# Kernel optimization log

Measured on AMD Instinct MI355X. Metric: run time of the kernel, lower is better.

Reference implementation:

```python
import jax, jax.numpy as jnp
import numpy as np

EPS = 1e-5  # torch BatchNorm1d default eps


def setup_inputs() -> dict:
    key = jax.random.key(0)
    ks = jax.random.split(key, 8)
    B, H, D, DO = 8192, 8, 512, 256
    return {
        "x_concepts_encoded": jax.random.normal(ks[0], (B, H, D), dtype=jnp.float32),
        "relevance_weights": jax.random.uniform(ks[1], (B, H), dtype=jnp.float32),
        "bn_gamma": jax.random.uniform(ks[2], (D,), dtype=jnp.float32) + 0.5,
        "bn_beta": jax.random.normal(ks[3], (D,), dtype=jnp.float32) * 0.1,
        "bn_mean": jax.random.normal(ks[4], (D,), dtype=jnp.float32) * 0.1,
        "bn_var": jax.random.uniform(ks[5], (D,), dtype=jnp.float32) + 0.5,
        "W": jax.random.normal(ks[6], (DO, D), dtype=jnp.float32) / np.sqrt(D),
        "b": jax.random.normal(ks[7], (DO,), dtype=jnp.float32) * 0.01,
    }


def reference(x_concepts_encoded, relevance_weights, bn_gamma, bn_beta, bn_mean, bn_var, W, b):
    B, H = relevance_weights.shape
    x = x_concepts_encoded.reshape(B * H, -1)            # [B*H, D]
    # BatchNorm1d (inference: running stats) fused as scale/shift
    inv = bn_gamma * jax.lax.rsqrt(bn_var + EPS)
    h = x * inv + (bn_beta - bn_mean * inv)              # [B*H, D]
    # Swish
    h = h * jax.nn.sigmoid(h)
    # Linear
    out = h @ W.T + b                                    # [B*H, DO]
    # relevance-weighted sum over heads
    out = jnp.einsum('bhd,bh->bd', out.reshape(B, H, -1), relevance_weights)
    return out
```

## Files before the change

### kernel.cpp

```cpp
#include <hip/hip_runtime.h>
#include <hip/hip_bf16.h>

#define NB 8192
#define NH 8
#define ND 512
#define NO 256
#define ROWS 32
#define TPB 512

typedef __attribute__((ext_vector_type(8))) short short8;
typedef __attribute__((ext_vector_type(4))) float f32x4;

__device__ __align__(16) ushort g_wb[NO * ND];

__device__ __forceinline__ ushort f2bf(float f) {
    union { float f; unsigned u; } v; v.f = f;
    unsigned u = v.u;
    unsigned r = u + 0x7FFFu + ((u >> 16) & 1u);
    return (ushort)(r >> 16);
}

__global__ __launch_bounds__(256) void wcvt_kernel(const float* __restrict__ W) {
    int i = (blockIdx.x * 256 + threadIdx.x) * 4;
    float4 w = *(const float4*)(W + i);
    ushort4 o;
    o.x = f2bf(w.x); o.y = f2bf(w.y); o.z = f2bf(w.z); o.w = f2bf(w.w);
    *(ushort4*)(g_wb + i) = o;
}

__device__ __forceinline__ float swishf(float h) {
    return h * __builtin_amdgcn_rcpf(1.0f + __expf(-h));
}

__global__ __launch_bounds__(TPB) void fused_kernel(
    const float* __restrict__ x, const float* __restrict__ rw,
    const float* __restrict__ gamma, const float* __restrict__ beta,
    const float* __restrict__ mean, const float* __restrict__ var,
    const float* __restrict__ bias, float* __restrict__ out)
{
    __shared__ __align__(16) ushort yl[ROWS * ND];
    __shared__ float rwl[ROWS * NH];

    const int tid = threadIdx.x;
    const int b0  = blockIdx.x * ROWS;
    const int d4  = tid & 127;
    const int rh  = tid >> 7;
    const int d   = d4 * 4;

    const int lane = tid & 63;
    const int wv   = tid >> 6;
    const int n0   = wv * 32;
    const int lr   = lane & 15;
    const int lk   = (lane >> 4) * 8;

    if (tid < 64)
        ((float4*)rwl)[tid] = ((const float4*)(rw + (size_t)b0 * NH))[tid];

    float4 g4 = *(const float4*)(gamma + d);
    float4 v4 = *(const float4*)(var   + d);
    float4 be = *(const float4*)(beta  + d);
    float4 me = *(const float4*)(mean  + d);
    const float ix = g4.x * rsqrtf(v4.x + 1e-5f);
    const float iy = g4.y * rsqrtf(v4.y + 1e-5f);
    const float iz = g4.z * rsqrtf(v4.z + 1e-5f);
    const float iw = g4.w * rsqrtf(v4.w + 1e-5f);
    const float ox = be.x - me.x * ix;
    const float oy = be.y - me.y * iy;
    const float oz = be.z - me.z * iz;
    const float ow = be.w - me.w * iw;

    __syncthreads();

    #pragma unroll
    for (int it = 0; it < 8; ++it) {
        const int rr = rh + it * 4;
        const float* xr = x + (size_t)(b0 + rr) * (NH * ND) + d;
        const float4 w0 = ((const float4*)(rwl + rr * NH))[0];
        const float4 w1 = ((const float4*)(rwl + rr * NH))[1];
        const float whv[NH] = {w0.x, w0.y, w0.z, w0.w, w1.x, w1.y, w1.z, w1.w};

        float ax = 0.f, ay = 0.f, az = 0.f, aw = 0.f;
        #pragma unroll
        for (int h = 0; h < NH; ++h) {
            float4 xa = *(const float4*)(xr + h * ND);
            const float wh = whv[h];
            ax += wh * swishf(xa.x * ix + ox);
            ay += wh * swishf(xa.y * iy + oy);
            az += wh * swishf(xa.z * iz + oz);
            aw += wh * swishf(xa.w * iw + ow);
        }
        const int addr = rr * 1024 + ((d * 2) ^ ((rr & 7) << 4));
        ushort4 o;
        o.x = f2bf(ax); o.y = f2bf(ay); o.z = f2bf(az); o.w = f2bf(aw);
        *(ushort4*)((char*)yl + addr) = o;
    }

    const ushort* wp = g_wb + (size_t)(n0 + lr) * ND + lk;
    short8 rb0[4], rb1[4];
    #pragma unroll
    for (int p = 0; p < 4; ++p) {
        rb0[p] = *(const short8*)(wp + p * 32);
        rb1[p] = *(const short8*)(wp + 16 * ND + p * 32);
    }
    __builtin_amdgcn_sched_barrier(0);
    __syncthreads();

    f32x4 acc00 = {0.f,0.f,0.f,0.f};
    f32x4 acc01 = {0.f,0.f,0.f,0.f};
    f32x4 acc10 = {0.f,0.f,0.f,0.f};
    f32x4 acc11 = {0.f,0.f,0.f,0.f};

    const char* ylb0 = (const char*)yl + lr * 1024;
    const char* ylb1 = (const char*)yl + (lr + 16) * 1024;
    const int swz = (lr & 7) << 4;

    #pragma unroll
    for (int ks = 0; ks < 16; ++ks) {
        short8 b0 = rb0[ks & 3];
        short8 b1 = rb1[ks & 3];
        if (ks + 4 < 16) {
            rb0[ks & 3] = *(const short8*)(wp + (ks + 4) * 32);
            rb1[ks & 3] = *(const short8*)(wp + 16 * ND + (ks + 4) * 32);
        }
        const int kb = (ks * 32 + lk) * 2;
        short8 a0 = *(const short8*)(ylb0 + (kb ^ swz));
        short8 a1 = *(const short8*)(ylb1 + (kb ^ swz));
        acc00 = __builtin_amdgcn_mfma_f32_16x16x32_bf16(a0, b0, acc00, 0, 0, 0);
        acc01 = __builtin_amdgcn_mfma_f32_16x16x32_bf16(a0, b1, acc01, 0, 0, 0);
        acc10 = __builtin_amdgcn_mfma_f32_16x16x32_bf16(a1, b0, acc10, 0, 0, 0);
        acc11 = __builtin_amdgcn_mfma_f32_16x16x32_bf16(a1, b1, acc11, 0, 0, 0);
    }

    const int rbase = (lane >> 4) * 4;
    float sw0[4], sw1[4];
    #pragma unroll
    for (int q = 0; q < 4; ++q) {
        const float* rp0 = rwl + (rbase + q) * NH;
        const float* rp1 = rwl + (16 + rbase + q) * NH;
        sw0[q] = ((rp0[0]+rp0[1]) + (rp0[2]+rp0[3])) + ((rp0[4]+rp0[5]) + (rp0[6]+rp0[7]));
        sw1[q] = ((rp1[0]+rp1[1]) + (rp1[2]+rp1[3])) + ((rp1[4]+rp1[5]) + (rp1[6]+rp1[7]));
    }
    f32x4 accs0[2] = {acc00, acc01};
    f32x4 accs1[2] = {acc10, acc11};
    #pragma unroll
    for (int nf = 0; nf < 2; ++nf) {
        const int col = n0 + nf * 16 + lr;
        const float bn = bias[col];
        #pragma unroll
        for (int q = 0; q < 4; ++q) {
            const int r = rbase + q;
            out[(size_t)(b0 + r) * NO + col]      = accs0[nf][q] + bn * sw0[q];
            out[(size_t)(b0 + 16 + r) * NO + col] = accs1[nf][q] + bn * sw1[q];
        }
    }
}

extern "C" void kernel_launch(void* const* d_in, const int* in_sizes, int n_in,
                              void* d_out, int out_size, void* d_ws, size_t ws_size,
                              hipStream_t stream) {
    const float* x     = (const float*)d_in[0];
    const float* rw    = (const float*)d_in[1];
    const float* gamma = (const float*)d_in[2];
    const float* beta  = (const float*)d_in[3];
    const float* mean  = (const float*)d_in[4];
    const float* var   = (const float*)d_in[5];
    const float* W     = (const float*)d_in[6];
    const float* bias  = (const float*)d_in[7];
    float* out = (float*)d_out;

    hipLaunchKernelGGL(wcvt_kernel, dim3((NO * ND) / 1024), dim3(256), 0, stream, W);
    hipLaunchKernelGGL(fused_kernel, dim3(NB / ROWS), dim3(TPB), 0, stream,
                       x, rw, gamma, beta, mean, var, bias, out);
}
```

Baseline: 38.24 us.

## Split block work into two half-row phases overlapping x loads with MFMA

Splits each block's 32 rows into two halves. The first 16 rows are reduced and multiplied, while global loads for the second half's x rows are already in flight before the first MFMA loop starts. The second half's swish and reduce and its own MFMA pass follow. The aim is to hide HBM latency for x behind the first GEMM, at the cost of reloading the W fragments, an extra barrier and higher register pressure from holding 16 prefetched float4s.

```diff
diff --git a/kernel.cpp b/kernel.cpp
--- a/kernel.cpp
+++ b/kernel.cpp
@@ -71,28 +71,37 @@
 
     __syncthreads();
 
-    #pragma unroll
-    for (int it = 0; it < 8; ++it) {
+#define COMPUTE_FROM(Xb, rr) do {                                           \
+    const float4 _w0 = ((const float4*)(rwl + (rr) * NH))[0];               \
+    const float4 _w1 = ((const float4*)(rwl + (rr) * NH))[1];               \
+    const float _whv[NH] = {_w0.x,_w0.y,_w0.z,_w0.w,_w1.x,_w1.y,_w1.z,_w1.w};\
+    float ax = 0.f, ay = 0.f, az = 0.f, aw = 0.f;                           \
+    _Pragma("unroll")                                                       \
+    for (int h = 0; h < NH; ++h) {                                          \
+        const float _wh = _whv[h];                                          \
+        ax += _wh * swishf(Xb[h].x * ix + ox);                              \
+        ay += _wh * swishf(Xb[h].y * iy + oy);                              \
+        az += _wh * swishf(Xb[h].z * iz + oz);                              \
+        aw += _wh * swishf(Xb[h].w * iw + ow);                              \
+    }                                                                       \
+    const int _addr = (rr) * 1024 + ((d * 2) ^ (((rr) & 7) << 4));          \
+    ushort4 _o;                                                             \
+    _o.x = f2bf(ax); _o.y = f2bf(ay); _o.z = f2bf(az); _o.w = f2bf(aw);     \
+    *(ushort4*)((char*)yl + _addr) = _o;                                    \
+} while (0)
+
+#define ISSUE(Xb, rr) do {                                                  \
+    const float* _xr = x + (size_t)(b0 + (rr)) * (NH * ND) + d;             \
+    _Pragma("unroll")                                                       \
+    for (int h = 0; h < NH; ++h) Xb[h] = *(const float4*)(_xr + h * ND);    \
+} while (0)
+
+    #pragma unroll
+    for (int it = 0; it < 4; ++it) {
         const int rr = rh + it * 4;
-        const float* xr = x + (size_t)(b0 + rr) * (NH * ND) + d;
-        const float4 w0 = ((const float4*)(rwl + rr * NH))[0];
-        const float4 w1 = ((const float4*)(rwl + rr * NH))[1];
-        const float whv[NH] = {w0.x, w0.y, w0.z, w0.w, w1.x, w1.y, w1.z, w1.w};
-
-        float ax = 0.f, ay = 0.f, az = 0.f, aw = 0.f;
-        #pragma unroll
-        for (int h = 0; h < NH; ++h) {
-            float4 xa = *(const float4*)(xr + h * ND);
-            const float wh = whv[h];
-            ax += wh * swishf(xa.x * ix + ox);
-            ay += wh * swishf(xa.y * iy + oy);
-            az += wh * swishf(xa.z * iz + oz);
-            aw += wh * swishf(xa.w * iw + ow);
-        }
-        const int addr = rr * 1024 + ((d * 2) ^ ((rr & 7) << 4));
-        ushort4 o;
-        o.x = f2bf(ax); o.y = f2bf(ay); o.z = f2bf(az); o.w = f2bf(aw);
-        *(ushort4*)((char*)yl + addr) = o;
+        float4 Xc[NH];
+        ISSUE(Xc, rr);
+        COMPUTE_FROM(Xc, rr);
     }
 
     const ushort* wp = g_wb + (size_t)(n0 + lr) * ND + lk;
@@ -102,16 +111,17 @@
         rb0[p] = *(const short8*)(wp + p * 32);
         rb1[p] = *(const short8*)(wp + 16 * ND + p * 32);
     }
+
+    float4 X0[NH], X1[NH];
+    ISSUE(X0, 16 + rh);
+    ISSUE(X1, 16 + rh + 4);
+
     __builtin_amdgcn_sched_barrier(0);
     __syncthreads();
 
-    f32x4 acc00 = {0.f,0.f,0.f,0.f};
-    f32x4 acc01 = {0.f,0.f,0.f,0.f};
-    f32x4 acc10 = {0.f,0.f,0.f,0.f};
-    f32x4 acc11 = {0.f,0.f,0.f,0.f};
-
+    f32x4 accA = {0.f,0.f,0.f,0.f};
+    f32x4 accB = {0.f,0.f,0.f,0.f};
     const char* ylb0 = (const char*)yl + lr * 1024;
-    const char* ylb1 = (const char*)yl + (lr + 16) * 1024;
     const int swz = (lr & 7) << 4;
 
     #pragma unroll
@@ -124,35 +134,82 @@
         }
         const int kb = (ks * 32 + lk) * 2;
         short8 a0 = *(const short8*)(ylb0 + (kb ^ swz));
+        accA = __builtin_amdgcn_mfma_f32_16x16x32_bf16(a0, b0, accA, 0, 0, 0);
+        accB = __builtin_amdgcn_mfma_f32_16x16x32_bf16(a0, b1, accB, 0, 0, 0);
+    }
+
+    const int rbase = (lane >> 4) * 4;
+    {
+        float sw0[4];
+        #pragma unroll
+        for (int q = 0; q < 4; ++q) {
+            const float* rp = rwl + (rbase + q) * NH;
+            sw0[q] = ((rp[0]+rp[1]) + (rp[2]+rp[3])) + ((rp[4]+rp[5]) + (rp[6]+rp[7]));
+        }
+        f32x4 accs[2] = {accA, accB};
+        #pragma unroll
+        for (int nf = 0; nf < 2; ++nf) {
+            const int col = n0 + nf * 16 + lr;
+            const float bn = bias[col];
+            #pragma unroll
+            for (int q = 0; q < 4; ++q)
+                out[(size_t)(b0 + rbase + q) * NO + col] = accs[nf][q] + bn * sw0[q];
+        }
+    }
+
+    COMPUTE_FROM(X0, 16 + rh);
+    ISSUE(X0, 16 + rh + 8);
+    COMPUTE_FROM(X1, 16 + rh + 4);
+    ISSUE(X1, 16 + rh + 12);
+    COMPUTE_FROM(X0, 16 + rh + 8);
+    COMPUTE_FROM(X1, 16 + rh + 12);
+
+    #pragma unroll
+    for (int p = 0; p < 4; ++p) {
+        rb0[p] = *(const short8*)(wp + p * 32);
+        rb1[p] = *(const short8*)(wp + 16 * ND + p * 32);
+    }
+    __builtin_amdgcn_sched_barrier(0);
+    __syncthreads();
+
+    f32x4 accC = {0.f,0.f,0.f,0.f};
+    f32x4 accD = {0.f,0.f,0.f,0.f};
+    const char* ylb1 = (const char*)yl + (lr + 16) * 1024;
+
+    #pragma unroll
+    for (int ks = 0; ks < 16; ++ks) {
+        short8 b0 = rb0[ks & 3];
+        short8 b1 = rb1[ks & 3];
+        if (ks + 4 < 16) {
+            rb0[ks & 3] = *(const short8*)(wp + (ks + 4) * 32);
+            rb1[ks & 3] = *(const short8*)(wp + 16 * ND + (ks + 4) * 32);
+        }
+        const int kb = (ks * 32 + lk) * 2;
         short8 a1 = *(const short8*)(ylb1 + (kb ^ swz));
-        acc00 = __builtin_amdgcn_mfma_f32_16x16x32_bf16(a0, b0, acc00, 0, 0, 0);
-        acc01 = __builtin_amdgcn_mfma_f32_16x16x32_bf16(a0, b1, acc01, 0, 0, 0);
-        acc10 = __builtin_amdgcn_mfma_f32_16x16x32_bf16(a1, b0, acc10, 0, 0, 0);
-        acc11 = __builtin_amdgcn_mfma_f32_16x16x32_bf16(a1, b1, acc11, 0, 0, 0);
-    }
-
-    const int rbase = (lane >> 4) * 4;
-    float sw0[4], sw1[4];
-    #pragma unroll
-    for (int q = 0; q < 4; ++q) {
-        const float* rp0 = rwl + (rbase + q) * NH;
-        const float* rp1 = rwl + (16 + rbase + q) * NH;
-        sw0[q] = ((rp0[0]+rp0[1]) + (rp0[2]+rp0[3])) + ((rp0[4]+rp0[5]) + (rp0[6]+rp0[7]));
-        sw1[q] = ((rp1[0]+rp1[1]) + (rp1[2]+rp1[3])) + ((rp1[4]+rp1[5]) + (rp1[6]+rp1[7]));
-    }
-    f32x4 accs0[2] = {acc00, acc01};
-    f32x4 accs1[2] = {acc10, acc11};
-    #pragma unroll
-    for (int nf = 0; nf < 2; ++nf) {
-        const int col = n0 + nf * 16 + lr;
-        const float bn = bias[col];
+        accC = __builtin_amdgcn_mfma_f32_16x16x32_bf16(a1, b0, accC, 0, 0, 0);
+        accD = __builtin_amdgcn_mfma_f32_16x16x32_bf16(a1, b1, accD, 0, 0, 0);
+    }
+
+    {
+        float sw1[4];
         #pragma unroll
         for (int q = 0; q < 4; ++q) {
-            const int r = rbase + q;
-            out[(size_t)(b0 + r) * NO + col]      = accs0[nf][q] + bn * sw0[q];
-            out[(size_t)(b0 + 16 + r) * NO + col] = accs1[nf][q] + bn * sw1[q];
-        }
-    }
+            const float* rp = rwl + (16 + rbase + q) * NH;
+            sw1[q] = ((rp[0]+rp[1]) + (rp[2]+rp[3])) + ((rp[4]+rp[5]) + (rp[6]+rp[7]));
+        }
+        f32x4 accs[2] = {accC, accD};
+        #pragma unroll
+        for (int nf = 0; nf < 2; ++nf) {
+            const int col = n0 + nf * 16 + lr;
+            const float bn = bias[col];
+            #pragma unroll
+            for (int q = 0; q < 4; ++q)
+                out[(size_t)(b0 + 16 + rbase + q) * NO + col] = accs[nf][q] + bn * sw1[q];
+        }
+    }
+
+#undef COMPUTE_FROM
+#undef ISSUE
 }
 
 extern "C" void kernel_launch(void* const* d_in, const int* in_sizes, int n_in,
```

After: 44.82 us. +17.2%, slower.
